# Kernel optimization log

Hardware: AMD Instinct MI355X
Metric: run time of the kernel (lower is better)

## Reference

```python
import jax, jax.numpy as jnp
import numpy as np

G = 512          # fine grid size
N_FINE = 150000  # target active fine voxels
THRESH = 0.8     # scn PPN Selection threshold


def _keys(c, g):
    c = c.astype(np.int64)
    return (c[:, 0] * g + c[:, 1]) * g + c[:, 2]


def _neighbors(coords, g):
    # coords: [N,3] int. Returns [N,27] neighbor indices; N == missing sentinel.
    keys = _keys(coords, g)
    order = np.argsort(keys)
    skeys = keys[order]
    N = coords.shape[0]
    offs = np.array([[dx, dy, dz] for dx in (-1, 0, 1) for dy in (-1, 0, 1) for dz in (-1, 0, 1)], np.int64)
    nbr = np.full((N, 27), N, np.int64)
    for k, o in enumerate(offs):
        nc = coords + o
        valid = np.all((nc >= 0) & (nc < g), axis=1)
        nk = _keys(np.clip(nc, 0, g - 1), g)
        pos = np.clip(np.searchsorted(skeys, nk), 0, N - 1)
        found = valid & (skeys[pos] == nk)
        nbr[:, k] = np.where(found, order[pos], N)
    return nbr


def _lookup(query, table, g):
    keys = _keys(table, g)
    order = np.argsort(keys)
    sk = keys[order]
    qk = _keys(query, g)
    pos = np.clip(np.searchsorted(sk, qk), 0, len(sk) - 1)
    return order[pos]


def setup_inputs() -> dict:
    rng = np.random.default_rng(0)
    pts = rng.integers(0, G, size=(2 * N_FINE, 3))
    fine = np.unique(pts, axis=0)[:N_FINE]              # stride-1 active sites
    mid = np.unique(fine // 4, axis=0)                  # stride-4 active sites
    coarse = np.unique(fine // 16, axis=0)              # stride-16 active sites
    N1, N2, N3 = coarse.shape[0], mid.shape[0], fine.shape[0]

    nbr1 = _neighbors(coarse, G // 16)
    nbr2 = _neighbors(mid, G // 4)
    nbr3 = _neighbors(fine, G)
    parent2 = _lookup(mid // 4, coarse, G // 16)        # middle voxel -> coarse parent
    parent3 = _lookup(fine // 4, mid, G // 4)           # fine voxel -> middle parent

    key = jax.random.key(0)
    ks = jax.random.split(key, 12)

    def w(k, shape):
        fan_in = shape[0] * shape[1]
        return jax.random.normal(k, shape, jnp.float32) / np.sqrt(fan_in)

    def coords4(c):  # prepend batch-id column (all batch 0) like get_spatial_locations
        return jnp.asarray(np.concatenate([c, np.zeros((c.shape[0], 1), c.dtype)], 1), jnp.int32)

    return {
        'feat1': jax.random.normal(ks[0], (N1, 80), jnp.float32),
        'feat2': jax.random.normal(ks[1], (N2, 48), jnp.float32),
        'feat3': jax.random.normal(ks[2], (N3, 16), jnp.float32),
        'W1': w(ks[3], (27, 80, 80)), 'W1s': w(ks[4], (27, 80, 2)),
        'W2': w(ks[5], (27, 48, 48)), 'W2s': w(ks[6], (27, 48, 2)),
        'W3': w(ks[7], (27, 16, 16)), 'W3p': w(ks[8], (27, 16, 3)),
        'W3s': w(ks[9], (27, 16, 2)), 'W3t': w(ks[10], (27, 16, 5)),
        'nbr1': jnp.asarray(nbr1, jnp.int32), 'nbr2': jnp.asarray(nbr2, jnp.int32),
        'nbr3': jnp.asarray(nbr3, jnp.int32),
        'parent2': jnp.asarray(parent2, jnp.int32), 'parent3': jnp.asarray(parent3, jnp.int32),
        'coords1': coords4(coarse), 'coords2': coords4(mid),
    }


def subconv(feat, nbr, W):
    # Submanifold 3^3 conv: out only at active sites; missing neighbors -> 0 (padded row).
    fp = jnp.concatenate([feat, jnp.zeros((1, feat.shape[1]), feat.dtype)], 0)
    g = fp[nbr]                               # [N, 27, Cin]
    return jnp.einsum('nkc,kcd->nd', g, W)    # [N, Cout]


def reference(feat1, feat2, feat3, W1, W1s, W2, W2s, W3, W3p, W3s, W3t,
              nbr1, nbr2, nbr3, parent2, parent3, coords1, coords2):
    # --- PPN1 on coarsest decoder features ---
    y = subconv(feat1, nbr1, W1)
    s1 = subconv(y, nbr1, W1s)                              # ppn1_scores [N1,2]
    mask1 = (jax.nn.softmax(s1, axis=1)[:, 1:] > THRESH).astype(feat1.dtype)  # Selection
    att1 = mask1[parent2]                                   # UnPooling x2: coarse -> middle
    # --- PPN2 on middle decoder features ---
    y2 = subconv(feat2 * att1, nbr2, W2)                    # Multiply then conv
    s2 = subconv(y2, nbr2, W2s)                             # ppn2_scores [N2,2]
    mask2 = (jax.nn.softmax(s2, axis=1)[:, 1:] > THRESH).astype(feat1.dtype)
    att2 = mask2[parent3]                                   # UnPooling x2: middle -> fine
    # --- PPN3 on finest decoder features ---
    z = subconv(feat3 * att2, nbr3, W3)
    pixel_pred = subconv(z, nbr3, W3p)                      # [N3,3]
    scores = subconv(z, nbr3, W3s)                          # [N3,2]
    ptype = subconv(z, nbr3, W3t)                           # [N3,5]
    points = jnp.concatenate([pixel_pred, scores, ptype], axis=1)
    ppn1 = jnp.concatenate([coords1.astype(jnp.float32), s1], axis=1)
    ppn2 = jnp.concatenate([coords2.astype(jnp.float32), s2], axis=1)
    return points, ppn1, ppn2, mask1, mask2
```

## Files before the change

kernel.cpp:

```cpp
#include <hip/hip_runtime.h>

typedef _Float16 f16;
typedef _Float16 f16x8 __attribute__((ext_vector_type(8)));
typedef float f32x4 __attribute__((ext_vector_type(4)));

#define LN4 1.3862943611198906f

__device__ __forceinline__ void gl_lds16(const void* g, void* l) {
    typedef unsigned int u32;
    __builtin_amdgcn_global_load_lds(
        (const __attribute__((address_space(1))) u32*)(g),
        (__attribute__((address_space(3))) u32*)(l), 16, 0, 0);
}

template<int CIN>
__global__ __launch_bounds__(256) void prep_wt(
    const float* __restrict__ W, f16* __restrict__ dst)
{
    const int RE = 2 * CIN;
    int total = CIN * 28 * CIN;
    for (int i = blockIdx.x * 256 + threadIdx.x; i < total; i += gridDim.x * 256) {
        int d = i / (28 * CIN);
        int rem = i - d * (28 * CIN);
        int tap = rem / CIN;
        int c = rem - tap * CIN;
        float v = (tap < 27) ? W[(size_t)(tap * CIN + c) * CIN + d] : 0.f;
        f16 h = (f16)v;
        size_t base = (size_t)d * (28 * RE) + (size_t)tap * RE;
        dst[base + c] = h;
        dst[base + CIN + c] = (f16)(v - (float)h);
    }
}

template<int CIN>
__global__ __launch_bounds__(256) void prep_gfrag(
    const float* __restrict__ Ws, f16* __restrict__ FG)
{
    constexpr int KB = (2 * CIN) / 32;
    int total = 2 * KB * 4 * 512;
    for (int i = blockIdx.x * 256 + threadIdx.x; i < total; i += gridDim.x * 256) {
        int j = i & 7;
        int lane = (i >> 3) & 63;
        int blk = i >> 9;
        int ct = blk & 3;
        int kbp = blk >> 2;
        int kb = kbp % KB;
        int pass = kbp / KB;
        int k = kb * 32 + ((lane >> 4) << 3) + j;
        int col = ct * 16 + (lane & 15);
        int c = (k < CIN) ? k : k - CIN;
        float w = 0.f;
        if (col < 54) {
            int t = col >> 1, jj = col & 1;
            w = Ws[((size_t)t * CIN + c) * 2 + jj];
        }
        f16 wh = (f16)w;
        FG[i] = (pass == 0) ? wh : ((k < CIN) ? (f16)(w - (float)wh) : (f16)0.f);
    }
}

template<int CIN>
__global__ __launch_bounds__(256) void split_gated(
    const float* __restrict__ f, const float* __restrict__ mask,
    const int* __restrict__ parent, f16* __restrict__ Fc, int N)
{
    int i = blockIdx.x * 256 + threadIdx.x;
    if (i >= (N + 1) * CIN) return;
    int n = i / CIN, c = i - n * CIN;
    float v = 0.f;
    if (n < N) {
        bool a = parent ? (mask[parent[n]] != 0.f) : true;
        v = a ? f[i] : 0.f;
    }
    f16 h = (f16)v;
    Fc[(size_t)n * (2 * CIN) + c] = h;
    Fc[(size_t)n * (2 * CIN) + CIN + c] = (f16)(v - (float)h);
}

__global__ __launch_bounds__(256) void gate_kernel(
    const float* __restrict__ mask, const int* __restrict__ parent,
    float* __restrict__ act, int N)
{
    int i = blockIdx.x * 256 + threadIdx.x;
    if (i < N) act[i] = mask[parent[i]];
}

template<bool FSRC>
__global__ __launch_bounds__(256) void expand_kernel(
    const void* __restrict__ src, const int* __restrict__ nbr,
    int* __restrict__ flag, int N)
{
    int m = blockIdx.x * 256 + threadIdx.x;
    if (m >= N) return;
    bool a = FSRC ? (((const float*)src)[m] != 0.f) : (((const int*)src)[m] != 0);
    if (!a) return;
    #pragma unroll 1
    for (int t = 0; t < 27; ++t) {
        int idx = nbr[(size_t)m * 27 + t];
        if (idx < N) flag[idx] = 1;
    }
}

__global__ __launch_bounds__(256) void compact_kernel(
    const int* __restrict__ flag, int* __restrict__ list,
    int* __restrict__ cnt, int N)
{
    int i = blockIdx.x * 256 + threadIdx.x;
    int lane = threadIdx.x & 63;
    bool f = (i < N) && (flag[i] != 0);
    unsigned long long m = __ballot(f);
    int base = 0;
    if (lane == 0 && m) base = atomicAdd(cnt, __popcll(m));
    base = __shfl(base, 0);
    if (f) list[base + __popcll(m & ((1ull << lane) - 1ull))] = i;
}

template<int CIN, int RS>
__global__ __launch_bounds__(256, RS == 1 ? 3 : 3) void conv_tile(
    const f16* __restrict__ F, const int* __restrict__ nbr,
    const f16* __restrict__ WT, f16* __restrict__ Y, int N, int nTiles)
{
    constexpr int RE = 2 * CIN;
    constexpr int KB = RE / 32;
    constexpr int CT = CIN / 16;
    constexpr int CPT = RE / 8;
    constexpr int CPR = 2 * CPT;
    constexpr int PB = CPR * 16;
    constexpr int BM = 64 * RS;
    __shared__ __align__(16) char BS[CIN * PB];

    const int t = threadIdx.x;
    const int lane = t & 63;
    const int l16 = lane & 15;
    const int quad = lane >> 4;
    const int wv = t >> 6;

    int q8 = (nTiles + 7) >> 3;
    int tile = (blockIdx.x & 7) * q8 + (blockIdx.x >> 3);
    if (tile >= nTiles) return;
    const int m0 = tile * BM;
    const int grow = m0 + wv * 16 + l16;

    f16x8 ahA[RS][KB], alA[RS][KB], ahB[RS][KB], alB[RS][KB];

    auto loadA = [&](int p, f16x8 (&ah)[RS][KB], f16x8 (&al)[RS][KB]) {
        #pragma unroll
        for (int rs = 0; rs < RS; ++rs) {
            int g = grow + rs * 64;
            int i0 = N, i1 = N;
            if (g < N) {
                i0 = nbr[(size_t)g * 27 + 2 * p];
                if (2 * p + 1 < 27) i1 = nbr[(size_t)g * 27 + 2 * p + 1];
            }
            #pragma unroll
            for (int kb = 0; kb < KB; ++kb) {
                int ko = kb * 32 + quad * 8;
                int ts = ko >= CIN;
                int c2 = ko - (ts ? CIN : 0);
                const f16* ap = F + (size_t)(ts ? i1 : i0) * RE + c2;
                ah[rs][kb] = *(const f16x8*)ap;
                al[rs][kb] = *(const f16x8*)(ap + CIN);
            }
        }
    };

    auto stageB = [&](int p) {
        for (int i = t; i < CIN * CPR; i += 256) {
            int d = i / CPR, cs = i - d * CPR;
            int c = (cs & ~7) | ((cs ^ d) & 7);
            int tp = c / CPT, cc = c - tp * CPT;
            gl_lds16((const char*)WT + (((size_t)d * 28 + 2 * p + tp) * RE + cc * 8) * 2,
                     BS + (size_t)i * 16);
        }
    };

    f32x4 acc[RS][CT];
    #pragma unroll
    for (int rs = 0; rs < RS; ++rs)
        #pragma unroll
        for (int ct = 0; ct < CT; ++ct) acc[rs][ct] = (f32x4){0.f, 0.f, 0.f, 0.f};

    auto compute = [&](f16x8 (&ah)[RS][KB], f16x8 (&al)[RS][KB]) {
        #pragma unroll
        for (int kb = 0; kb < KB; ++kb) {
            int ko = kb * 32 + quad * 8;
            int ts = ko >= CIN;
            int c2 = ko - (ts ? CIN : 0);
            int ch = ts * CPT + c2 / 8;
            int chl = ch + CIN / 8;
            #pragma unroll
            for (int ct = 0; ct < CT; ++ct) {
                int drow = ct * 16 + l16;
                int sb = (ch & ~7) | ((ch ^ drow) & 7);
                int sbl = (chl & ~7) | ((chl ^ drow) & 7);
                f16x8 bh = *(const f16x8*)(BS + drow * PB + sb * 16);
                f16x8 bl = *(const f16x8*)(BS + drow * PB + sbl * 16);
                #pragma unroll
                for (int rs = 0; rs < RS; ++rs) {
                    acc[rs][ct] = __builtin_amdgcn_mfma_f32_16x16x32_f16(ah[rs][kb], bh, acc[rs][ct], 0, 0, 0);
                    acc[rs][ct] = __builtin_amdgcn_mfma_f32_16x16x32_f16(al[rs][kb], bh, acc[rs][ct], 0, 0, 0);
                    acc[rs][ct] = __builtin_amdgcn_mfma_f32_16x16x32_f16(ah[rs][kb], bl, acc[rs][ct], 0, 0, 0);
                }
            }
        }
    };

    loadA(0, ahA, alA);
    #pragma unroll 1
    for (int p = 0; p < 14; p += 2) {
        __syncthreads();
        stageB(p);
        loadA(p + 1, ahB, alB);
        __syncthreads();
        compute(ahA, alA);

        __syncthreads();
        stageB(p + 1);
        if (p + 2 < 14) loadA(p + 2, ahA, alA);
        __syncthreads();
        compute(ahB, alB);
    }

    #pragma unroll
    for (int rs = 0; rs < RS; ++rs) {
        #pragma unroll
        for (int ct = 0; ct < CT; ++ct) {
            #pragma unroll
            for (int r = 0; r < 4; ++r) {
                int row = m0 + rs * 64 + wv * 16 + quad * 4 + r;
                if (row < N) {
                    int d = ct * 16 + l16;
                    float v = acc[rs][ct][r];
                    f16 h = (f16)v;
                    Y[(size_t)row * RE + d] = h;
                    Y[(size_t)row * RE + CIN + d] = (f16)(v - (float)h);
                }
            }
        }
    }
}

template<int CIN>
__global__ __launch_bounds__(256) void gemm_P(
    const f16* __restrict__ Y, const f16* __restrict__ FG,
    float* __restrict__ P, int N, int nTiles)
{
    constexpr int RE = 2 * CIN;
    constexpr int KB = RE / 32;

    const int t = threadIdx.x;
    const int lane = t & 63;
    const int l16 = lane & 15;
    const int quad = lane >> 4;
    const int wv = t >> 6;

    int q8 = (nTiles + 7) >> 3;
    int tile = (blockIdx.x & 7) * q8 + (blockIdx.x >> 3);
    if (tile >= nTiles) return;
    const int m0 = tile * 64;
    const int grow = m0 + wv * 16 + l16;
    const int arow = (grow < N) ? grow : N;
    const f16* ar = Y + (size_t)arow * RE;

    f32x4 acc[4];
    #pragma unroll
    for (int ct = 0; ct < 4; ++ct) acc[ct] = (f32x4){0.f, 0.f, 0.f, 0.f};

    #pragma unroll
    for (int kb = 0; kb < KB; ++kb) {
        f16x8 a = *(const f16x8*)(ar + kb * 32 + quad * 8);
        #pragma unroll
        for (int ct = 0; ct < 4; ++ct) {
            f16x8 b = *(const f16x8*)(FG + ((size_t)((0 * KB + kb) * 4 + ct)) * 512 + lane * 8);
            acc[ct] = __builtin_amdgcn_mfma_f32_16x16x32_f16(a, b, acc[ct], 0, 0, 0);
        }
        #pragma unroll
        for (int ct = 0; ct < 4; ++ct) {
            f16x8 b = *(const f16x8*)(FG + ((size_t)((1 * KB + kb) * 4 + ct)) * 512 + lane * 8);
            acc[ct] = __builtin_amdgcn_mfma_f32_16x16x32_f16(a, b, acc[ct], 0, 0, 0);
        }
    }

    #pragma unroll
    for (int ct = 0; ct < 4; ++ct) {
        int col = ct * 16 + l16;
        if (col < 54) {
            #pragma unroll
            for (int r = 0; r < 4; ++r) {
                int row = m0 + wv * 16 + quad * 4 + r;
                if (row < N) P[(size_t)row * 54 + col] = acc[ct][r];
            }
        }
    }
}

__global__ __launch_bounds__(256) void finalize_gather(
    const int* __restrict__ coords, const float* __restrict__ P,
    const int* __restrict__ nbr, float* __restrict__ ppn,
    float* __restrict__ mask, int N)
{
    int n = blockIdx.x * 256 + threadIdx.x;
    if (n >= N) return;
    float s0 = 0.f, s1 = 0.f;
    #pragma unroll
    for (int t = 0; t < 27; ++t) {
        int idx = nbr[(size_t)n * 27 + t];
        if (idx < N) {
            float2 v = *(const float2*)(P + (size_t)idx * 54 + 2 * t);
            s0 += v.x; s1 += v.y;
        }
    }
    ppn[(size_t)n * 6 + 0] = (float)coords[(size_t)n * 4 + 0];
    ppn[(size_t)n * 6 + 1] = (float)coords[(size_t)n * 4 + 1];
    ppn[(size_t)n * 6 + 2] = (float)coords[(size_t)n * 4 + 2];
    ppn[(size_t)n * 6 + 3] = (float)coords[(size_t)n * 4 + 3];
    ppn[(size_t)n * 6 + 4] = s0;
    ppn[(size_t)n * 6 + 5] = s1;
    mask[n] = (s1 - s0 > LN4) ? 1.0f : 0.0f;
}

__global__ __launch_bounds__(256) void lvl3_z_compute(
    const float* __restrict__ feat3, const int* __restrict__ nbr3,
    const float* __restrict__ act, const float* __restrict__ W3,
    float* __restrict__ z, const int* __restrict__ list,
    const int* __restrict__ cnt, int N)
{
    const int lane = threadIdx.x & 63;
    const int wid0 = (blockIdx.x * 256 + threadIdx.x) >> 6;
    const int nw = (gridDim.x * 256) >> 6;
    const int count = *cnt;
    const int c = lane;

    for (int w = wid0; w < count; w += nw) {
        const int n = list[w];
        int ld = N;
        if (lane < 27) ld = nbr3[(size_t)n * 27 + lane];
        bool valid = (lane < 27) && (ld < N);
        float a = valid ? act[ld] : 0.f;
        unsigned long long m = __ballot(a != 0.f);

        float acc = 0.f;
        while (m) {
            int t = __ffsll(m) - 1; m &= m - 1;
            int idx = __shfl(ld, t);
            const float4* f4 = (const float4*)(feat3 + (size_t)idx * 16);
            const float* wgt = W3 + (size_t)t * 256;
            #pragma unroll
            for (int q = 0; q < 4; ++q) {
                float4 fv = f4[q];
                if (c < 16) {
                    acc += fv.x * wgt[(4 * q + 0) * 16 + c];
                    acc += fv.y * wgt[(4 * q + 1) * 16 + c];
                    acc += fv.z * wgt[(4 * q + 2) * 16 + c];
                    acc += fv.w * wgt[(4 * q + 3) * 16 + c];
                }
            }
        }
        if (lane < 16) z[(size_t)n * 16 + lane] = acc;
    }
}

__global__ __launch_bounds__(256) void lvl3_pts_compute(
    const float* __restrict__ z, const int* __restrict__ zflag,
    const int* __restrict__ nbr3,
    const float* __restrict__ Wp, const float* __restrict__ Ws,
    const float* __restrict__ Wt, float* __restrict__ points,
    const int* __restrict__ list, const int* __restrict__ cnt, int N)
{
    const int lane = threadIdx.x & 63;
    const int wid0 = (blockIdx.x * 256 + threadIdx.x) >> 6;
    const int nw = (gridDim.x * 256) >> 6;
    const int count = *cnt;
    const int c = lane;

    for (int w = wid0; w < count; w += nw) {
        const int n = list[w];
        int ld = N;
        if (lane < 27) ld = nbr3[(size_t)n * 27 + lane];
        bool valid = (lane < 27) && (ld < N);
        int zf = valid ? zflag[ld] : 0;
        unsigned long long m = __ballot(zf != 0);

        float acc = 0.f;
        while (m) {
            int t = __ffsll(m) - 1; m &= m - 1;
            int idx = __shfl(ld, t);
            const float4* z4 = (const float4*)(z + (size_t)idx * 16);
            #pragma unroll
            for (int q = 0; q < 4; ++q) {
                float4 zv = z4[q];
                if (c < 10) {
                    #pragma unroll
                    for (int j = 0; j < 4; ++j) {
                        int k = 4 * q + j;
                        int kc = t * 16 + k;
                        float wv = (c < 3) ? Wp[(size_t)kc * 3 + c]
                                 : (c < 5) ? Ws[(size_t)kc * 2 + (c - 3)]
                                           : Wt[(size_t)kc * 5 + (c - 5)];
                        float zj = (j == 0) ? zv.x : (j == 1) ? zv.y : (j == 2) ? zv.z : zv.w;
                        acc += zj * wv;
                    }
                }
            }
        }
        if (lane < 10) points[(size_t)n * 10 + lane] = acc;
    }
}

extern "C" void kernel_launch(void* const* d_in, const int* in_sizes, int n_in,
                              void* d_out, int out_size, void* d_ws, size_t ws_size,
                              hipStream_t stream)
{
    const float* feat1 = (const float*)d_in[0];
    const float* feat2 = (const float*)d_in[1];
    const float* feat3 = (const float*)d_in[2];
    const float* W1    = (const float*)d_in[3];
    const float* W1s   = (const float*)d_in[4];
    const float* W2    = (const float*)d_in[5];
    const float* W2s   = (const float*)d_in[6];
    const float* W3    = (const float*)d_in[7];
    const float* W3p   = (const float*)d_in[8];
    const float* W3s   = (const float*)d_in[9];
    const float* W3t   = (const float*)d_in[10];
    const int* nbr1    = (const int*)d_in[11];
    const int* nbr2    = (const int*)d_in[12];
    const int* nbr3    = (const int*)d_in[13];
    const int* parent2 = (const int*)d_in[14];
    const int* parent3 = (const int*)d_in[15];
    const int* coords1 = (const int*)d_in[16];
    const int* coords2 = (const int*)d_in[17];

    const int N1 = in_sizes[0] / 80;
    const int N2 = in_sizes[1] / 48;
    const int N3 = in_sizes[2] / 16;

    float* out = (float*)d_out;
    float* o_points = out;
    float* o_ppn1   = o_points + (size_t)N3 * 10;
    float* o_ppn2   = o_ppn1 + (size_t)N1 * 6;
    float* o_mask1  = o_ppn2 + (size_t)N2 * 6;
    float* o_mask2  = o_mask1 + (size_t)N1;

    char* wp = (char*)d_ws;
    auto alloc = [&](size_t bytes) -> char* {
        char* r = wp; wp += (bytes + 255) & ~(size_t)255; return r;
    };
    auto A256 = [](size_t b) { return (b + 255) & ~(size_t)255; };

    f16*   WT1 = (f16*)alloc((size_t)80 * 28 * 160 * 2);
    f16*   WT2 = (f16*)alloc((size_t)48 * 28 * 96 * 2);
    f16*   FG1 = (f16*)alloc((size_t)2 * 5 * 4 * 512 * 2);
    f16*   FG2 = (f16*)alloc((size_t)2 * 3 * 4 * 512 * 2);
    float* act3 = (float*)alloc((size_t)N3 * 4);
    int*   cnts = (int*)alloc(2 * 4);

    size_t fa1 = (size_t)(N1 + 1) * 320, fa2 = (size_t)(N2 + 1) * 192;
    size_t pmax = (size_t)(N1 > N2 ? N1 : N2) * 216 + 256;
    size_t szFaP = fa1 > fa2 ? fa1 : fa2; if (pmax > szFaP) szFaP = pmax;
    char* FaP = alloc(szFaP);
    f16*   Fa = (f16*)FaP;
    float* P  = (float*)FaP;

    size_t l3b = 4 * A256((size_t)N3 * 4) + A256((size_t)N3 * 16 * 4);
    size_t szY = fa1 > fa2 ? fa1 : fa2; if (l3b > szY) szY = l3b;
    char* Yu = alloc(szY);
    f16* Y = (f16*)Yu;
    char* q3 = Yu;
    int*   flagz = (int*)q3; q3 += A256((size_t)N3 * 4);
    int*   listz = (int*)q3; q3 += A256((size_t)N3 * 4);
    int*   flagp = (int*)q3; q3 += A256((size_t)N3 * 4);
    int*   listp = (int*)q3; q3 += A256((size_t)N3 * 4);
    float* zbuf  = (float*)q3;

    auto cdiv = [](long long a, long long b) { return (int)((a + b - 1) / b); };

    hipMemsetAsync(cnts, 0, 2 * 4, stream);
    hipMemsetAsync(o_points, 0, (size_t)N3 * 10 * 4, stream);

    prep_wt<80><<<700, 256, 0, stream>>>(W1, WT1);
    prep_wt<48><<<cdiv(48 * 28 * 48, 256), 256, 0, stream>>>(W2, WT2);
    prep_gfrag<80><<<80, 256, 0, stream>>>(W1s, FG1);
    prep_gfrag<48><<<48, 256, 0, stream>>>(W2s, FG2);

    {
        int Tc = cdiv(N1, 64);
        dim3 gc(8 * cdiv(Tc, 8));
        split_gated<80><<<cdiv((size_t)(N1 + 1) * 80, 256), 256, 0, stream>>>(
            feat1, nullptr, nullptr, Fa, N1);
        conv_tile<80, 1><<<gc, 256, 0, stream>>>(Fa, nbr1, WT1, Y, N1, Tc);
        gemm_P<80><<<gc, 256, 0, stream>>>(Y, FG1, P, N1, Tc);
        finalize_gather<<<cdiv(N1, 256), 256, 0, stream>>>(
            coords1, P, nbr1, o_ppn1, o_mask1, N1);
    }

    {
        int Tc = cdiv(N2, 128);
        dim3 gc(8 * cdiv(Tc, 8));
        int Tg = cdiv(N2, 64);
        dim3 gg(8 * cdiv(Tg, 8));
        split_gated<48><<<cdiv((size_t)(N2 + 1) * 48, 256), 256, 0, stream>>>(
            feat2, o_mask1, parent2, Fa, N2);
        conv_tile<48, 2><<<gc, 256, 0, stream>>>(Fa, nbr2, WT2, Y, N2, Tc);
        gemm_P<48><<<gg, 256, 0, stream>>>(Y, FG2, P, N2, Tg);
        finalize_gather<<<cdiv(N2, 256), 256, 0, stream>>>(
            coords2, P, nbr2, o_ppn2, o_mask2, N2);
    }

    hipMemsetAsync(flagz, 0, (size_t)N3 * 4, stream);
    hipMemsetAsync(flagp, 0, (size_t)N3 * 4, stream);
    hipMemsetAsync(zbuf, 0, (size_t)N3 * 16 * 4, stream);
    gate_kernel<<<cdiv(N3, 256), 256, 0, stream>>>(o_mask2, parent3, act3, N3);
    expand_kernel<true><<<cdiv(N3, 256), 256, 0, stream>>>(act3, nbr3, flagz, N3);
    compact_kernel<<<cdiv(N3, 256), 256, 0, stream>>>(flagz, listz, &cnts[0], N3);
    lvl3_z_compute<<<2048, 256, 0, stream>>>(feat3, nbr3, act3, W3, zbuf,
                                             listz, &cnts[0], N3);
    expand_kernel<false><<<cdiv(N3, 256), 256, 0, stream>>>(flagz, nbr3, flagp, N3);
    compact_kernel<<<cdiv(N3, 256), 256, 0, stream>>>(flagp, listp, &cnts[1], N3);
    lvl3_pts_compute<<<2048, 256, 0, stream>>>(zbuf, flagz, nbr3, W3p, W3s, W3t,
                                               o_points, listp, &cnts[1], N3);
}
```

Baseline: 371.7 us.

## Restructure conv tiles to taps-per-phase, fuse gate with expand kernel

The conv_tile template now takes a taps-per-phase parameter instead of a row-stacking factor. Level 2 uses 64-row tiles with 4 taps per K phase, which halves the phase count and barriers while giving more blocks. B-staging source addresses are precomputed and advanced by a fixed stride. gate_kernel and the first expand_kernel are fused into one launch, which drops a kernel and a read of act3. Level 2 now gets less weight reuse per block and uses more LDS per block, which may reduce occupancy.

```diff
diff --git a/kernel.cpp b/kernel.cpp
--- a/kernel.cpp
+++ b/kernel.cpp
@@ -77,23 +77,30 @@
     Fc[(size_t)n * (2 * CIN) + CIN + c] = (f16)(v - (float)h);
 }
 
-__global__ __launch_bounds__(256) void gate_kernel(
+__global__ __launch_bounds__(256) void gate_expand(
     const float* __restrict__ mask, const int* __restrict__ parent,
-    float* __restrict__ act, int N)
-{
-    int i = blockIdx.x * 256 + threadIdx.x;
-    if (i < N) act[i] = mask[parent[i]];
-}
-
-template<bool FSRC>
-__global__ __launch_bounds__(256) void expand_kernel(
-    const void* __restrict__ src, const int* __restrict__ nbr,
+    const int* __restrict__ nbr, float* __restrict__ act,
     int* __restrict__ flag, int N)
 {
     int m = blockIdx.x * 256 + threadIdx.x;
     if (m >= N) return;
-    bool a = FSRC ? (((const float*)src)[m] != 0.f) : (((const int*)src)[m] != 0);
-    if (!a) return;
+    float a = mask[parent[m]];
+    act[m] = a;
+    if (a == 0.f) return;
+    #pragma unroll 1
+    for (int t = 0; t < 27; ++t) {
+        int idx = nbr[(size_t)m * 27 + t];
+        if (idx < N) flag[idx] = 1;
+    }
+}
+
+__global__ __launch_bounds__(256) void expand_kernel(
+    const int* __restrict__ src, const int* __restrict__ nbr,
+    int* __restrict__ flag, int N)
+{
+    int m = blockIdx.x * 256 + threadIdx.x;
+    if (m >= N) return;
+    if (src[m] == 0) return;
     #pragma unroll 1
     for (int t = 0; t < 27; ++t) {
         int idx = nbr[(size_t)m * 27 + t];
@@ -115,18 +122,21 @@
     if (f) list[base + __popcll(m & ((1ull << lane) - 1ull))] = i;
 }
 
-template<int CIN, int RS>
-__global__ __launch_bounds__(256, RS == 1 ? 3 : 3) void conv_tile(
+template<int CIN, int TPP>
+__global__ __launch_bounds__(256, 3) void conv_tile(
     const f16* __restrict__ F, const int* __restrict__ nbr,
     const f16* __restrict__ WT, f16* __restrict__ Y, int N, int nTiles)
 {
-    constexpr int RE = 2 * CIN;
-    constexpr int KB = RE / 32;
-    constexpr int CT = CIN / 16;
+    constexpr int RE  = 2 * CIN;
     constexpr int CPT = RE / 8;
-    constexpr int CPR = 2 * CPT;
-    constexpr int PB = CPR * 16;
-    constexpr int BM = 64 * RS;
+    constexpr int CPR = TPP * CPT;
+    constexpr int PB  = CPR * 16;
+    constexpr int KB  = (TPP * CIN) / 32;
+    constexpr int CT  = CIN / 16;
+    constexpr int NCH = CIN * CPR;
+    constexpr int NIT = (NCH + 255) / 256;
+    constexpr int NPH = (27 + TPP - 1) / TPP;
+    constexpr int STEP = TPP * RE * 2;
     __shared__ __align__(16) char BS[CIN * PB];
 
     const int t = threadIdx.x;
@@ -138,54 +148,65 @@
     int q8 = (nTiles + 7) >> 3;
     int tile = (blockIdx.x & 7) * q8 + (blockIdx.x >> 3);
     if (tile >= nTiles) return;
-    const int m0 = tile * BM;
+    const int m0 = tile * 64;
     const int grow = m0 + wv * 16 + l16;
-
-    f16x8 ahA[RS][KB], alA[RS][KB], ahB[RS][KB], alB[RS][KB];
-
-    auto loadA = [&](int p, f16x8 (&ah)[RS][KB], f16x8 (&al)[RS][KB]) {
-        #pragma unroll
-        for (int rs = 0; rs < RS; ++rs) {
-            int g = grow + rs * 64;
-            int i0 = N, i1 = N;
-            if (g < N) {
-                i0 = nbr[(size_t)g * 27 + 2 * p];
-                if (2 * p + 1 < 27) i1 = nbr[(size_t)g * 27 + 2 * p + 1];
+    const int* nrow = nbr + (size_t)(grow < N ? grow : 0) * 27;
+
+    f16x8 ahA[KB], alA[KB], ahB[KB], alB[KB];
+
+    auto loadA = [&](int p, f16x8 (&ah)[KB], f16x8 (&al)[KB]) {
+        int j0 = N, j1 = N, j2 = N, j3 = N;
+        if (grow < N) {
+            int t0 = TPP * p;
+            j0 = nrow[t0];
+            if (t0 + 1 < 27) j1 = nrow[t0 + 1];
+            if constexpr (TPP == 4) {
+                if (t0 + 2 < 27) j2 = nrow[t0 + 2];
+                if (t0 + 3 < 27) j3 = nrow[t0 + 3];
             }
-            #pragma unroll
-            for (int kb = 0; kb < KB; ++kb) {
-                int ko = kb * 32 + quad * 8;
-                int ts = ko >= CIN;
-                int c2 = ko - (ts ? CIN : 0);
-                const f16* ap = F + (size_t)(ts ? i1 : i0) * RE + c2;
-                ah[rs][kb] = *(const f16x8*)ap;
-                al[rs][kb] = *(const f16x8*)(ap + CIN);
-            }
-        }
-    };
-
-    auto stageB = [&](int p) {
-        for (int i = t; i < CIN * CPR; i += 256) {
-            int d = i / CPR, cs = i - d * CPR;
-            int c = (cs & ~7) | ((cs ^ d) & 7);
-            int tp = c / CPT, cc = c - tp * CPT;
-            gl_lds16((const char*)WT + (((size_t)d * 28 + 2 * p + tp) * RE + cc * 8) * 2,
-                     BS + (size_t)i * 16);
-        }
-    };
-
-    f32x4 acc[RS][CT];
-    #pragma unroll
-    for (int rs = 0; rs < RS; ++rs)
-        #pragma unroll
-        for (int ct = 0; ct < CT; ++ct) acc[rs][ct] = (f32x4){0.f, 0.f, 0.f, 0.f};
-
-    auto compute = [&](f16x8 (&ah)[RS][KB], f16x8 (&al)[RS][KB]) {
+        }
         #pragma unroll
         for (int kb = 0; kb < KB; ++kb) {
             int ko = kb * 32 + quad * 8;
-            int ts = ko >= CIN;
-            int c2 = ko - (ts ? CIN : 0);
+            int ts = ko / CIN;
+            int c2 = ko - ts * CIN;
+            int ii = (ts == 0) ? j0 : (ts == 1) ? j1 : (ts == 2) ? j2 : j3;
+            const f16* ap = F + (size_t)ii * RE + c2;
+            ah[kb] = *(const f16x8*)ap;
+            al[kb] = *(const f16x8*)(ap + CIN);
+        }
+    };
+
+    const char* ssrc[NIT];
+    #pragma unroll
+    for (int it = 0; it < NIT; ++it) {
+        int i = t + it * 256;
+        int iv = (i < NCH) ? i : 0;
+        int d = iv / CPR, cs = iv - d * CPR;
+        int c = (cs & ~7) | ((cs ^ d) & 7);
+        int tp = c / CPT, cc = c - tp * CPT;
+        ssrc[it] = (const char*)WT + (((size_t)d * 28 + tp) * RE + cc * 8) * 2;
+    }
+
+    auto stageB = [&]() {
+        #pragma unroll
+        for (int it = 0; it < NIT; ++it) {
+            int i = t + it * 256;
+            if (i < NCH) gl_lds16(ssrc[it], BS + (size_t)i * 16);
+            ssrc[it] += STEP;
+        }
+    };
+
+    f32x4 acc[CT];
+    #pragma unroll
+    for (int ct = 0; ct < CT; ++ct) acc[ct] = (f32x4){0.f, 0.f, 0.f, 0.f};
+
+    auto compute = [&](f16x8 (&ah)[KB], f16x8 (&al)[KB]) {
+        #pragma unroll
+        for (int kb = 0; kb < KB; ++kb) {
+            int ko = kb * 32 + quad * 8;
+            int ts = ko / CIN;
+            int c2 = ko - ts * CIN;
             int ch = ts * CPT + c2 / 8;
             int chl = ch + CIN / 8;
             #pragma unroll
@@ -195,46 +216,42 @@
                 int sbl = (chl & ~7) | ((chl ^ drow) & 7);
                 f16x8 bh = *(const f16x8*)(BS + drow * PB + sb * 16);
                 f16x8 bl = *(const f16x8*)(BS + drow * PB + sbl * 16);
-                #pragma unroll
-                for (int rs = 0; rs < RS; ++rs) {
-                    acc[rs][ct] = __builtin_amdgcn_mfma_f32_16x16x32_f16(ah[rs][kb], bh, acc[rs][ct], 0, 0, 0);
-                    acc[rs][ct] = __builtin_amdgcn_mfma_f32_16x16x32_f16(al[rs][kb], bh, acc[rs][ct], 0, 0, 0);
-                    acc[rs][ct] = __builtin_amdgcn_mfma_f32_16x16x32_f16(ah[rs][kb], bl, acc[rs][ct], 0, 0, 0);
-                }
+                acc[ct] = __builtin_amdgcn_mfma_f32_16x16x32_f16(ah[kb], bh, acc[ct], 0, 0, 0);
+                acc[ct] = __builtin_amdgcn_mfma_f32_16x16x32_f16(al[kb], bh, acc[ct], 0, 0, 0);
+                acc[ct] = __builtin_amdgcn_mfma_f32_16x16x32_f16(ah[kb], bl, acc[ct], 0, 0, 0);
             }
         }
     };
 
     loadA(0, ahA, alA);
     #pragma unroll 1
-    for (int p = 0; p < 14; p += 2) {
+    for (int p = 0; ; p += 2) {
         __syncthreads();
-        stageB(p);
-        loadA(p + 1, ahB, alB);
+        stageB();
+        bool hasB = (p + 1 < NPH);
+        if (hasB) loadA(p + 1, ahB, alB);
         __syncthreads();
         compute(ahA, alA);
-
+        if (!hasB) break;
         __syncthreads();
-        stageB(p + 1);
-        if (p + 2 < 14) loadA(p + 2, ahA, alA);
+        stageB();
+        if (p + 2 < NPH) loadA(p + 2, ahA, alA);
         __syncthreads();
         compute(ahB, alB);
-    }
-
-    #pragma unroll
-    for (int rs = 0; rs < RS; ++rs) {
+        if (p + 2 >= NPH) break;
+    }
+
+    #pragma unroll
+    for (int ct = 0; ct < CT; ++ct) {
         #pragma unroll
-        for (int ct = 0; ct < CT; ++ct) {
-            #pragma unroll
-            for (int r = 0; r < 4; ++r) {
-                int row = m0 + rs * 64 + wv * 16 + quad * 4 + r;
-                if (row < N) {
-                    int d = ct * 16 + l16;
-                    float v = acc[rs][ct][r];
-                    f16 h = (f16)v;
-                    Y[(size_t)row * RE + d] = h;
-                    Y[(size_t)row * RE + CIN + d] = (f16)(v - (float)h);
-                }
+        for (int r = 0; r < 4; ++r) {
+            int row = m0 + wv * 16 + quad * 4 + r;
+            if (row < N) {
+                int d = ct * 16 + l16;
+                float v = acc[ct][r];
+                f16 h = (f16)v;
+                Y[(size_t)row * RE + d] = h;
+                Y[(size_t)row * RE + CIN + d] = (f16)(v - (float)h);
             }
         }
     }
@@ -487,21 +504,19 @@
         dim3 gc(8 * cdiv(Tc, 8));
         split_gated<80><<<cdiv((size_t)(N1 + 1) * 80, 256), 256, 0, stream>>>(
             feat1, nullptr, nullptr, Fa, N1);
-        conv_tile<80, 1><<<gc, 256, 0, stream>>>(Fa, nbr1, WT1, Y, N1, Tc);
+        conv_tile<80, 2><<<gc, 256, 0, stream>>>(Fa, nbr1, WT1, Y, N1, Tc);
         gemm_P<80><<<gc, 256, 0, stream>>>(Y, FG1, P, N1, Tc);
         finalize_gather<<<cdiv(N1, 256), 256, 0, stream>>>(
             coords1, P, nbr1, o_ppn1, o_mask1, N1);
     }
 
     {
-        int Tc = cdiv(N2, 128);
+        int Tc = cdiv(N2, 64);
         dim3 gc(8 * cdiv(Tc, 8));
-        int Tg = cdiv(N2, 64);
-        dim3 gg(8 * cdiv(Tg, 8));
         split_gated<48><<<cdiv((size_t)(N2 + 1) * 48, 256), 256, 0, stream>>>(
             feat2, o_mask1, parent2, Fa, N2);
-        conv_tile<48, 2><<<gc, 256, 0, stream>>>(Fa, nbr2, WT2, Y, N2, Tc);
-        gemm_P<48><<<gg, 256, 0, stream>>>(Y, FG2, P, N2, Tg);
+        conv_tile<48, 4><<<gc, 256, 0, stream>>>(Fa, nbr2, WT2, Y, N2, Tc);
+        gemm_P<48><<<gc, 256, 0, stream>>>(Y, FG2, P, N2, Tc);
         finalize_gather<<<cdiv(N2, 256), 256, 0, stream>>>(
             coords2, P, nbr2, o_ppn2, o_mask2, N2);
     }
@@ -509,12 +524,12 @@
     hipMemsetAsync(flagz, 0, (size_t)N3 * 4, stream);
     hipMemsetAsync(flagp, 0, (size_t)N3 * 4, stream);
     hipMemsetAsync(zbuf, 0, (size_t)N3 * 16 * 4, stream);
-    gate_kernel<<<cdiv(N3, 256), 256, 0, stream>>>(o_mask2, parent3, act3, N3);
-    expand_kernel<true><<<cdiv(N3, 256), 256, 0, stream>>>(act3, nbr3, flagz, N3);
+    gate_expand<<<cdiv(N3, 256), 256, 0, stream>>>(o_mask2, parent3, nbr3,
+                                                   act3, flagz, N3);
     compact_kernel<<<cdiv(N3, 256), 256, 0, stream>>>(flagz, listz, &cnts[0], N3);
     lvl3_z_compute<<<2048, 256, 0, stream>>>(feat3, nbr3, act3, W3, zbuf,
                                              listz, &cnts[0], N3);
-    expand_kernel<false><<<cdiv(N3, 256), 256, 0, stream>>>(flagz, nbr3, flagp, N3);
+    expand_kernel<<<cdiv(N3, 256), 256, 0, stream>>>(flagz, nbr3, flagp, N3);
     compact_kernel<<<cdiv(N3, 256), 256, 0, stream>>>(flagp, listp, &cnts[1], N3);
     lvl3_pts_compute<<<2048, 256, 0, stream>>>(zbuf, flagz, nbr3, W3p, W3s, W3t,
                                                o_points, listp, &cnts[1], N3);
```

Result: slower. 446.3 us (+20.1%).
